# Kernel tuning notes

Measured on AMD Instinct MI355X. Metric: run time of the kernel, lower is better.

## Reference

```python
import jax, jax.numpy as jnp
import numpy as np

VOCAB, D, S, W, B = 32000, 768, 512, 300, 64
LMAX = 4  # max chars per word (spans are 1-3 chars)


def setup_inputs() -> dict:
    key = jax.random.key(0)
    k1, k2, k3, k4 = jax.random.split(key, 4)
    ernie_output = jax.random.normal(k1, (B, S, D), dtype=jnp.float32)
    word_embedding = jax.random.normal(k2, (VOCAB, D), dtype=jnp.float32)
    # structured word_index: (word_id, char_start, char_end) with contiguous spans
    lengths = jax.random.randint(k3, (B, W), 1, LMAX)  # 1..3 chars per word
    starts = 1 + jnp.concatenate(
        [jnp.zeros((B, 1), jnp.int32), jnp.cumsum(lengths, axis=1)[:, :-1]], axis=1
    ).astype(jnp.int32)
    ends = starts + lengths.astype(jnp.int32)  # tail words exceed S -> fallback path
    word_ids = jax.random.randint(k4, (B, W), 0, VOCAB, dtype=jnp.int32)
    word_index = jnp.stack([word_ids, starts, ends], axis=-1)  # (B, W, 3)
    return {"ernie_output": ernie_output, "word_embedding": word_embedding,
            "word_index": word_index}


def reference(ernie_output, word_embedding, word_index):
    Bb, Ss, Dd = ernie_output.shape
    Ww = word_index.shape[1]
    wid = word_index[..., 0]    # (B, W)
    st = word_index[..., 1]
    en = word_index[..., 2]
    span = en - st

    we = word_embedding[wid]                        # (B, W, D) query / fallback emb
    pos = st[..., None] + jnp.arange(LMAX)          # (B, W, LMAX)
    pos_c = jnp.clip(pos, 0, Ss - 1)
    chars = ernie_output[jnp.arange(Bb)[:, None, None], pos_c]  # (B, W, LMAX, D)

    # masked softmax attention pooling over the char span (len==1 reduces to copy)
    mask = jnp.arange(LMAX)[None, None, :] < jnp.maximum(span, 1)[..., None]
    scores = jnp.einsum('bwd,bwld->bwl', we, chars)
    scores = jnp.where(mask, scores, -jnp.inf)
    attn = jax.nn.softmax(scores, axis=-1)
    pooled = jnp.einsum('bwl,bwld->bwd', attn, chars)  # (B, W, D)

    in_range = en < Ss
    normal = jnp.where(in_range[..., None], pooled, we)

    # break semantics: first word with end<S and span<=0 fills positions j.. with
    # that word's embedding
    brk = in_range & (span <= 0)                   # (B, W)
    has_brk = jnp.any(brk, axis=1)
    first = jnp.where(has_brk, jnp.argmax(brk, axis=1), Ww)  # (B,)
    fill_id = wid[jnp.arange(Bb), jnp.clip(first, 0, Ww - 1)]
    fill = word_embedding[fill_id]                 # (B, D)
    jidx = jnp.arange(Ww)[None, :]
    out = jnp.where((jidx >= first[:, None])[..., None], fill[:, None, :], normal)
    return out
```

## Files before the change

### kernel.cpp

```cpp
#include <hip/hip_runtime.h>
#include <math.h>

#define VOCAB 32000
#define D 768
#define S 512
#define W 300
#define B 64
#define LMAX 4

typedef float f32x4 __attribute__((ext_vector_type(4)));

__global__ __launch_bounds__(64) void find_first_kernel(
    const int* __restrict__ word_index,
    int* __restrict__ first_out,
    int* __restrict__ fill_id_out)
{
    const int b = blockIdx.x;
    const int lane = threadIdx.x;
    int my_first = W;
    for (int w = lane; w < W; w += 64) {
        const int base = (b * W + w) * 3;
        const int st = word_index[base + 1];
        const int en = word_index[base + 2];
        if (en < S && (en - st) <= 0) my_first = min(my_first, w);
    }
    #pragma unroll
    for (int off = 32; off > 0; off >>= 1)
        my_first = min(my_first, __shfl_xor(my_first, off));
    if (lane == 0) {
        first_out[b] = my_first;
        const int fw = min(my_first, W - 1);
        fill_id_out[b] = word_index[(b * W + fw) * 3 + 0];
    }
}

__device__ __forceinline__ float wave_bcast_sum(float p) {
    #pragma unroll
    for (int off = 32; off > 0; off >>= 1) p += __shfl_xor(p, off);
    return p;
}

__global__ __launch_bounds__(256) void pool_kernel(
    const float* __restrict__ ernie,
    const float* __restrict__ emb,
    const int*   __restrict__ word_index,
    const int*   __restrict__ first_arr,
    const int*   __restrict__ fill_arr,
    float* __restrict__ out)
{
    int gwave = (int)((blockIdx.x * blockDim.x + threadIdx.x) >> 6);
    gwave = __builtin_amdgcn_readfirstlane(gwave);
    const int lane = threadIdx.x & 63;

    const int b = gwave / W;
    const int w = gwave - b * W;

    const int base = gwave * 3;
    const int wid = word_index[base + 0];
    const int st  = word_index[base + 1];
    const int en  = word_index[base + 2];

    f32x4* __restrict__ outp = (f32x4*)(out + (size_t)gwave * D);

    if (w >= first_arr[b]) {
        const f32x4* src = (const f32x4*)(emb + (size_t)fill_arr[b] * D);
        #pragma unroll
        for (int k = 0; k < 3; k++)
            __builtin_nontemporal_store(src[lane + 64 * k], &outp[lane + 64 * k]);
        return;
    }

    const f32x4* wep = (const f32x4*)(emb + (size_t)wid * D);
    f32x4 we0 = wep[lane], we1 = wep[lane + 64], we2 = wep[lane + 128];

    if (en >= S) {
        __builtin_nontemporal_store(we0, &outp[lane]);
        __builtin_nontemporal_store(we1, &outp[lane + 64]);
        __builtin_nontemporal_store(we2, &outp[lane + 128]);
        return;
    }

    const int span_eff = min(max(en - st, 1), LMAX);
    const f32x4* erow = (const f32x4*)(ernie + (size_t)b * S * D);

    float m = -INFINITY, denom = 0.f;
    f32x4 acc0 = 0.f, acc1 = 0.f, acc2 = 0.f;

    int p0 = min(max(st, 0), S - 1);
    f32x4 c0 = erow[p0 * 192 + lane];
    f32x4 c1 = erow[p0 * 192 + lane + 64];
    f32x4 c2 = erow[p0 * 192 + lane + 128];

    #pragma unroll
    for (int l = 0; l < LMAX; ++l) {
        if (l >= span_eff) break;
        f32x4 n0, n1, n2;
        if (l + 1 < span_eff) {
            int pn = min(max(st + l + 1, 0), S - 1);
            n0 = erow[pn * 192 + lane];
            n1 = erow[pn * 192 + lane + 64];
            n2 = erow[pn * 192 + lane + 128];
        } else {
            n0 = c0; n1 = c1; n2 = c2;
        }
        f32x4 pv = c0 * we0 + c1 * we1 + c2 * we2;
        float p = pv.x + pv.y + pv.z + pv.w;
        p = wave_bcast_sum(p);
        float mn = fmaxf(m, p);
        float scale = expf(m - mn);
        float e = expf(p - mn);
        denom = denom * scale + e;
        acc0 = acc0 * scale + e * c0;
        acc1 = acc1 * scale + e * c1;
        acc2 = acc2 * scale + e * c2;
        m = mn;
        c0 = n0; c1 = n1; c2 = n2;
    }

    const float inv = 1.f / denom;
    __builtin_nontemporal_store(acc0 * inv, &outp[lane]);
    __builtin_nontemporal_store(acc1 * inv, &outp[lane + 64]);
    __builtin_nontemporal_store(acc2 * inv, &outp[lane + 128]);
}

extern "C" void kernel_launch(void* const* d_in, const int* in_sizes, int n_in,
                              void* d_out, int out_size, void* d_ws, size_t ws_size,
                              hipStream_t stream) {
    const float* ernie      = (const float*)d_in[0];
    const float* emb        = (const float*)d_in[1];
    const int*   word_index = (const int*)d_in[2];
    float* out = (float*)d_out;

    int* first_arr = (int*)d_ws;
    int* fill_arr  = first_arr + B;

    find_first_kernel<<<B, 64, 0, stream>>>(word_index, first_arr, fill_arr);

    const int total_waves = B * W;
    const int grid = total_waves / 4;
    pool_kernel<<<grid, 256, 0, stream>>>(ernie, emb, word_index,
                                          first_arr, fill_arr, out);
}
```

Baseline: 228.4 us.

## Process four words per wavefront with batched embedding row loads

Each wavefront now handles four consecutive words instead of one. It loads all four query or fill embedding rows up front, then pools or copies each word in turn, and the grid shrinks by four. The goal is more outstanding memory requests per wave and amortised index and metadata loads. The cost is higher register pressure and fewer waves in flight. Softmax exponentials switch to the fast __expf intrinsic.

```diff
diff --git a/kernel.cpp b/kernel.cpp
--- a/kernel.cpp
+++ b/kernel.cpp
@@ -7,6 +7,7 @@
 #define W 300
 #define B 64
 #define LMAX 4
+#define WPW 4
 
 typedef float f32x4 __attribute__((ext_vector_type(4)));
 
@@ -40,7 +41,7 @@
     return p;
 }
 
-__global__ __launch_bounds__(256) void pool_kernel(
+__global__ __launch_bounds__(256, 4) void pool_kernel(
     const float* __restrict__ ernie,
     const float* __restrict__ emb,
     const int*   __restrict__ word_index,
@@ -48,79 +49,91 @@
     const int*   __restrict__ fill_arr,
     float* __restrict__ out)
 {
-    int gwave = (int)((blockIdx.x * blockDim.x + threadIdx.x) >> 6);
-    gwave = __builtin_amdgcn_readfirstlane(gwave);
+    int gw = (int)((blockIdx.x * blockDim.x + threadIdx.x) >> 6);
+    gw = __builtin_amdgcn_readfirstlane(gw);
     const int lane = threadIdx.x & 63;
 
-    const int b = gwave / W;
-    const int w = gwave - b * W;
+    const int b  = gw / (W / WPW);
+    const int w0 = (gw - b * (W / WPW)) * WPW;
 
-    const int base = gwave * 3;
-    const int wid = word_index[base + 0];
-    const int st  = word_index[base + 1];
-    const int en  = word_index[base + 2];
+    const int base = (b * W + w0) * 3;
+    int wid[WPW], st[WPW], en[WPW];
+    #pragma unroll
+    for (int i = 0; i < WPW; ++i) {
+        wid[i] = word_index[base + 3 * i + 0];
+        st[i]  = word_index[base + 3 * i + 1];
+        en[i]  = word_index[base + 3 * i + 2];
+    }
+    const int first  = first_arr[b];
+    const int fillid = fill_arr[b];
 
-    f32x4* __restrict__ outp = (f32x4*)(out + (size_t)gwave * D);
-
-    if (w >= first_arr[b]) {
-        const f32x4* src = (const f32x4*)(emb + (size_t)fill_arr[b] * D);
-        #pragma unroll
-        for (int k = 0; k < 3; k++)
-            __builtin_nontemporal_store(src[lane + 64 * k], &outp[lane + 64 * k]);
-        return;
+    const f32x4* __restrict__ embv = (const f32x4*)emb;
+    f32x4 we[WPW][3];
+    #pragma unroll
+    for (int i = 0; i < WPW; ++i) {
+        const int rid = (w0 + i >= first) ? fillid : wid[i];
+        const f32x4* rp = embv + (size_t)rid * 192;
+        we[i][0] = rp[lane];
+        we[i][1] = rp[lane + 64];
+        we[i][2] = rp[lane + 128];
     }
 
-    const f32x4* wep = (const f32x4*)(emb + (size_t)wid * D);
-    f32x4 we0 = wep[lane], we1 = wep[lane + 64], we2 = wep[lane + 128];
-
-    if (en >= S) {
-        __builtin_nontemporal_store(we0, &outp[lane]);
-        __builtin_nontemporal_store(we1, &outp[lane + 64]);
-        __builtin_nontemporal_store(we2, &outp[lane + 128]);
-        return;
-    }
-
-    const int span_eff = min(max(en - st, 1), LMAX);
-    const f32x4* erow = (const f32x4*)(ernie + (size_t)b * S * D);
-
-    float m = -INFINITY, denom = 0.f;
-    f32x4 acc0 = 0.f, acc1 = 0.f, acc2 = 0.f;
-
-    int p0 = min(max(st, 0), S - 1);
-    f32x4 c0 = erow[p0 * 192 + lane];
-    f32x4 c1 = erow[p0 * 192 + lane + 64];
-    f32x4 c2 = erow[p0 * 192 + lane + 128];
+    f32x4* __restrict__ outp0 = (f32x4*)out + (size_t)(b * W + w0) * 192;
+    const f32x4* __restrict__ erow = (const f32x4*)ernie + (size_t)b * S * 192;
 
     #pragma unroll
-    for (int l = 0; l < LMAX; ++l) {
-        if (l >= span_eff) break;
-        f32x4 n0, n1, n2;
-        if (l + 1 < span_eff) {
-            int pn = min(max(st + l + 1, 0), S - 1);
-            n0 = erow[pn * 192 + lane];
-            n1 = erow[pn * 192 + lane + 64];
-            n2 = erow[pn * 192 + lane + 128];
-        } else {
-            n0 = c0; n1 = c1; n2 = c2;
+    for (int i = 0; i < WPW; ++i) {
+        f32x4* __restrict__ outp = outp0 + (size_t)i * 192;
+        const bool do_pool = (w0 + i < first) && (en[i] < S);
+
+        if (!do_pool) {
+            __builtin_nontemporal_store(we[i][0], &outp[lane]);
+            __builtin_nontemporal_store(we[i][1], &outp[lane + 64]);
+            __builtin_nontemporal_store(we[i][2], &outp[lane + 128]);
+            continue;
         }
-        f32x4 pv = c0 * we0 + c1 * we1 + c2 * we2;
-        float p = pv.x + pv.y + pv.z + pv.w;
-        p = wave_bcast_sum(p);
-        float mn = fmaxf(m, p);
-        float scale = expf(m - mn);
-        float e = expf(p - mn);
-        denom = denom * scale + e;
-        acc0 = acc0 * scale + e * c0;
-        acc1 = acc1 * scale + e * c1;
-        acc2 = acc2 * scale + e * c2;
-        m = mn;
-        c0 = n0; c1 = n1; c2 = n2;
+
+        const int span_eff = min(max(en[i] - st[i], 1), LMAX);
+
+        float m = -INFINITY, denom = 0.f;
+        f32x4 acc0 = 0.f, acc1 = 0.f, acc2 = 0.f;
+
+        const int p0 = min(max(st[i], 0), S - 1);
+        f32x4 c0 = erow[p0 * 192 + lane];
+        f32x4 c1 = erow[p0 * 192 + lane + 64];
+        f32x4 c2 = erow[p0 * 192 + lane + 128];
+
+        #pragma unroll
+        for (int l = 0; l < LMAX; ++l) {
+            if (l >= span_eff) break;
+            f32x4 n0, n1, n2;
+            if (l + 1 < span_eff) {
+                const int pn = min(max(st[i] + l + 1, 0), S - 1);
+                n0 = erow[pn * 192 + lane];
+                n1 = erow[pn * 192 + lane + 64];
+                n2 = erow[pn * 192 + lane + 128];
+            } else {
+                n0 = c0; n1 = c1; n2 = c2;
+            }
+            f32x4 pv = c0 * we[i][0] + c1 * we[i][1] + c2 * we[i][2];
+            float p = pv.x + pv.y + pv.z + pv.w;
+            p = wave_bcast_sum(p);
+            const float mn = fmaxf(m, p);
+            const float scale = __expf(m - mn);
+            const float e = __expf(p - mn);
+            denom = denom * scale + e;
+            acc0 = acc0 * scale + e * c0;
+            acc1 = acc1 * scale + e * c1;
+            acc2 = acc2 * scale + e * c2;
+            m = mn;
+            c0 = n0; c1 = n1; c2 = n2;
+        }
+
+        const float inv = 1.f / denom;
+        __builtin_nontemporal_store(acc0 * inv, &outp[lane]);
+        __builtin_nontemporal_store(acc1 * inv, &outp[lane + 64]);
+        __builtin_nontemporal_store(acc2 * inv, &outp[lane + 128]);
     }
-
-    const float inv = 1.f / denom;
-    __builtin_nontemporal_store(acc0 * inv, &outp[lane]);
-    __builtin_nontemporal_store(acc1 * inv, &outp[lane + 64]);
-    __builtin_nontemporal_store(acc2 * inv, &outp[lane + 128]);
 }
 
 extern "C" void kernel_launch(void* const* d_in, const int* in_sizes, int n_in,
@@ -136,8 +149,7 @@
 
     find_first_kernel<<<B, 64, 0, stream>>>(word_index, first_arr, fill_arr);
 
-    const int total_waves = B * W;
-    const int grid = total_waves / 4;
+    const int grid = (B * W) / (WPW * 4);
     pool_kernel<<<grid, 256, 0, stream>>>(ernie, emb, word_index,
                                           first_arr, fill_arr, out);
 }
```

Measured after the change: 231.9 us. About the same (+1.6%).

## Precompute per-word descriptors and issue all span loads before a two-pass softmax

Applied to the files above, without the earlier changes.

The prep kernel now emits one int4 descriptor per word (row id, ernie row offset, span, mode), so the pool kernel resolves the fill, fallback and pool cases with a single load instead of reading word_index and the per-batch arrays. The pool kernel issues every char-row load up front with nontemporal hints and computes the scores together. It then does a single max/exp softmax with batched shuffle reductions, replacing the serial online-softmax loop. This exposes more memory-level parallelism and shortens dependency chains, at the cost of more registers, a serial 64-thread prep pass writing descriptors, and fast __expf.

```diff
diff --git a/kernel.cpp b/kernel.cpp
--- a/kernel.cpp
+++ b/kernel.cpp
@@ -10,117 +10,135 @@
 
 typedef float f32x4 __attribute__((ext_vector_type(4)));
 
-__global__ __launch_bounds__(64) void find_first_kernel(
+__global__ __launch_bounds__(64) void prep_kernel(
     const int* __restrict__ word_index,
-    int* __restrict__ first_out,
-    int* __restrict__ fill_id_out)
+    int4* __restrict__ desc)
 {
     const int b = blockIdx.x;
     const int lane = threadIdx.x;
+
     int my_first = W;
     for (int w = lane; w < W; w += 64) {
         const int base = (b * W + w) * 3;
         const int st = word_index[base + 1];
         const int en = word_index[base + 2];
-        if (en < S && (en - st) <= 0) my_first = min(my_first, w);
+        if (en < S && en <= st) my_first = min(my_first, w);
     }
     #pragma unroll
     for (int off = 32; off > 0; off >>= 1)
         my_first = min(my_first, __shfl_xor(my_first, off));
-    if (lane == 0) {
-        first_out[b] = my_first;
-        const int fw = min(my_first, W - 1);
-        fill_id_out[b] = word_index[(b * W + fw) * 3 + 0];
+    const int first = my_first;
+
+    const int fw = min(first, W - 1);
+    const int fillid = word_index[(b * W + fw) * 3 + 0];
+
+    for (int w = lane; w < W; w += 64) {
+        const int base = (b * W + w) * 3;
+        const int wid = word_index[base + 0];
+        const int st  = word_index[base + 1];
+        const int en  = word_index[base + 2];
+        int4 d;
+        if (w >= first) {
+            d.x = fillid; d.y = 0; d.z = 0; d.w = 0;
+        } else if (en >= S) {
+            d.x = wid; d.y = 0; d.z = 0; d.w = 0;
+        } else {
+            const int p0 = min(max(st, 0), S - 1);
+            d.x = wid;
+            d.y = b * S + p0;
+            d.z = min(max(en - st, 1), LMAX);
+            d.w = 1;
+        }
+        desc[b * W + w] = d;
     }
-}
-
-__device__ __forceinline__ float wave_bcast_sum(float p) {
-    #pragma unroll
-    for (int off = 32; off > 0; off >>= 1) p += __shfl_xor(p, off);
-    return p;
 }
 
 __global__ __launch_bounds__(256) void pool_kernel(
     const float* __restrict__ ernie,
     const float* __restrict__ emb,
-    const int*   __restrict__ word_index,
-    const int*   __restrict__ first_arr,
-    const int*   __restrict__ fill_arr,
+    const int4* __restrict__ desc,
     float* __restrict__ out)
 {
-    int gwave = (int)((blockIdx.x * blockDim.x + threadIdx.x) >> 6);
-    gwave = __builtin_amdgcn_readfirstlane(gwave);
+    int gw = (int)((blockIdx.x * blockDim.x + threadIdx.x) >> 6);
+    gw = __builtin_amdgcn_readfirstlane(gw);
     const int lane = threadIdx.x & 63;
 
-    const int b = gwave / W;
-    const int w = gwave - b * W;
+    const int4 d = desc[gw];
 
-    const int base = gwave * 3;
-    const int wid = word_index[base + 0];
-    const int st  = word_index[base + 1];
-    const int en  = word_index[base + 2];
+    f32x4* __restrict__ outp = (f32x4*)out + (size_t)gw * 192;
+    const f32x4* __restrict__ rp = (const f32x4*)emb + (size_t)d.x * 192;
 
-    f32x4* __restrict__ outp = (f32x4*)(out + (size_t)gwave * D);
-
-    if (w >= first_arr[b]) {
-        const f32x4* src = (const f32x4*)(emb + (size_t)fill_arr[b] * D);
-        #pragma unroll
-        for (int k = 0; k < 3; k++)
-            __builtin_nontemporal_store(src[lane + 64 * k], &outp[lane + 64 * k]);
+    if (d.w == 0) {
+        __builtin_nontemporal_store(rp[lane],       &outp[lane]);
+        __builtin_nontemporal_store(rp[lane + 64],  &outp[lane + 64]);
+        __builtin_nontemporal_store(rp[lane + 128], &outp[lane + 128]);
         return;
     }
 
-    const f32x4* wep = (const f32x4*)(emb + (size_t)wid * D);
-    f32x4 we0 = wep[lane], we1 = wep[lane + 64], we2 = wep[lane + 128];
+    const int span = d.z;
+    const f32x4* __restrict__ cb = (const f32x4*)ernie + (size_t)d.y * 192;
 
-    if (en >= S) {
-        __builtin_nontemporal_store(we0, &outp[lane]);
-        __builtin_nontemporal_store(we1, &outp[lane + 64]);
-        __builtin_nontemporal_store(we2, &outp[lane + 128]);
-        return;
+    f32x4 we0 = rp[lane], we1 = rp[lane + 64], we2 = rp[lane + 128];
+
+    f32x4 c[LMAX][3];
+    c[0][0] = __builtin_nontemporal_load(&cb[lane]);
+    c[0][1] = __builtin_nontemporal_load(&cb[lane + 64]);
+    c[0][2] = __builtin_nontemporal_load(&cb[lane + 128]);
+    if (span > 1) {
+        c[1][0] = __builtin_nontemporal_load(&cb[192 + lane]);
+        c[1][1] = __builtin_nontemporal_load(&cb[192 + lane + 64]);
+        c[1][2] = __builtin_nontemporal_load(&cb[192 + lane + 128]);
+    }
+    if (span > 2) {
+        c[2][0] = __builtin_nontemporal_load(&cb[384 + lane]);
+        c[2][1] = __builtin_nontemporal_load(&cb[384 + lane + 64]);
+        c[2][2] = __builtin_nontemporal_load(&cb[384 + lane + 128]);
+    }
+    if (span > 3) {
+        c[3][0] = __builtin_nontemporal_load(&cb[576 + lane]);
+        c[3][1] = __builtin_nontemporal_load(&cb[576 + lane + 64]);
+        c[3][2] = __builtin_nontemporal_load(&cb[576 + lane + 128]);
     }
 
-    const int span_eff = min(max(en - st, 1), LMAX);
-    const f32x4* erow = (const f32x4*)(ernie + (size_t)b * S * D);
-
-    float m = -INFINITY, denom = 0.f;
-    f32x4 acc0 = 0.f, acc1 = 0.f, acc2 = 0.f;
-
-    int p0 = min(max(st, 0), S - 1);
-    f32x4 c0 = erow[p0 * 192 + lane];
-    f32x4 c1 = erow[p0 * 192 + lane + 64];
-    f32x4 c2 = erow[p0 * 192 + lane + 128];
+    f32x4 pv0 = c[0][0] * we0 + c[0][1] * we1 + c[0][2] * we2;
+    float s0 = pv0.x + pv0.y + pv0.z + pv0.w;
+    float s1 = -INFINITY, s2 = -INFINITY, s3 = -INFINITY;
+    if (span > 1) {
+        f32x4 pv = c[1][0] * we0 + c[1][1] * we1 + c[1][2] * we2;
+        s1 = pv.x + pv.y + pv.z + pv.w;
+    }
+    if (span > 2) {
+        f32x4 pv = c[2][0] * we0 + c[2][1] * we1 + c[2][2] * we2;
+        s2 = pv.x + pv.y + pv.z + pv.w;
+    }
+    if (span > 3) {
+        f32x4 pv = c[3][0] * we0 + c[3][1] * we1 + c[3][2] * we2;
+        s3 = pv.x + pv.y + pv.z + pv.w;
+    }
 
     #pragma unroll
-    for (int l = 0; l < LMAX; ++l) {
-        if (l >= span_eff) break;
-        f32x4 n0, n1, n2;
-        if (l + 1 < span_eff) {
-            int pn = min(max(st + l + 1, 0), S - 1);
-            n0 = erow[pn * 192 + lane];
-            n1 = erow[pn * 192 + lane + 64];
-            n2 = erow[pn * 192 + lane + 128];
-        } else {
-            n0 = c0; n1 = c1; n2 = c2;
-        }
-        f32x4 pv = c0 * we0 + c1 * we1 + c2 * we2;
-        float p = pv.x + pv.y + pv.z + pv.w;
-        p = wave_bcast_sum(p);
-        float mn = fmaxf(m, p);
-        float scale = expf(m - mn);
-        float e = expf(p - mn);
-        denom = denom * scale + e;
-        acc0 = acc0 * scale + e * c0;
-        acc1 = acc1 * scale + e * c1;
-        acc2 = acc2 * scale + e * c2;
-        m = mn;
-        c0 = n0; c1 = n1; c2 = n2;
+    for (int off = 32; off > 0; off >>= 1) {
+        s0 += __shfl_xor(s0, off);
+        s1 += __shfl_xor(s1, off);
+        s2 += __shfl_xor(s2, off);
+        s3 += __shfl_xor(s3, off);
     }
 
-    const float inv = 1.f / denom;
-    __builtin_nontemporal_store(acc0 * inv, &outp[lane]);
-    __builtin_nontemporal_store(acc1 * inv, &outp[lane + 64]);
-    __builtin_nontemporal_store(acc2 * inv, &outp[lane + 128]);
+    const float mx = fmaxf(fmaxf(s0, s1), fmaxf(s2, s3));
+    const float e0 = __expf(s0 - mx);
+    const float e1 = __expf(s1 - mx);
+    const float e2 = __expf(s2 - mx);
+    const float e3 = __expf(s3 - mx);
+    const float inv = 1.f / (e0 + e1 + e2 + e3);
+
+    f32x4 a0 = e0 * c[0][0], a1 = e0 * c[0][1], a2 = e0 * c[0][2];
+    if (span > 1) { a0 += e1 * c[1][0]; a1 += e1 * c[1][1]; a2 += e1 * c[1][2]; }
+    if (span > 2) { a0 += e2 * c[2][0]; a1 += e2 * c[2][1]; a2 += e2 * c[2][2]; }
+    if (span > 3) { a0 += e3 * c[3][0]; a1 += e3 * c[3][1]; a2 += e3 * c[3][2]; }
+
+    __builtin_nontemporal_store(a0 * inv, &outp[lane]);
+    __builtin_nontemporal_store(a1 * inv, &outp[lane + 64]);
+    __builtin_nontemporal_store(a2 * inv, &outp[lane + 128]);
 }
 
 extern "C" void kernel_launch(void* const* d_in, const int* in_sizes, int n_in,
@@ -131,13 +149,10 @@
     const int*   word_index = (const int*)d_in[2];
     float* out = (float*)d_out;
 
-    int* first_arr = (int*)d_ws;
-    int* fill_arr  = first_arr + B;
+    int4* desc = (int4*)d_ws;
 
-    find_first_kernel<<<B, 64, 0, stream>>>(word_index, first_arr, fill_arr);
+    prep_kernel<<<B, 64, 0, stream>>>(word_index, desc);
 
-    const int total_waves = B * W;
-    const int grid = total_waves / 4;
-    pool_kernel<<<grid, 256, 0, stream>>>(ernie, emb, word_index,
-                                          first_arr, fill_arr, out);
+    const int grid = (B * W) / 4;
+    pool_kernel<<<grid, 256, 0, stream>>>(ernie, emb, desc, out);
 }
```

After: 222.0 us. 1.03x faster.
